# Performance work log

Hardware: AMD Instinct MI355X
Metric: run time of the kernel (lower is better)

## Reference

```python
import jax, jax.numpy as jnp
import numpy as np

SEQ, B, IN, HID = 512, 64, 1024, 1024


def setup_inputs() -> dict:
    key = jax.random.key(0)
    ks = jax.random.split(key, 9)
    scale = 1.0 / np.sqrt(IN + HID)  # ~torch Linear init range
    def lin(k):
        kw, kb = jax.random.split(k)
        W = jax.random.uniform(kw, (IN + HID, HID), jnp.float32, -scale, scale)
        b = jax.random.uniform(kb, (HID,), jnp.float32, -scale, scale)
        return W, b
    W_f, b_f = lin(ks[0])
    W_i, b_i = lin(ks[1])
    W_o, b_o = lin(ks[2])
    W_c, b_c = lin(ks[3])
    x = jax.random.normal(ks[4], (SEQ, B, IN), jnp.float32)
    return {"x": x, "W_f": W_f, "b_f": b_f, "W_i": W_i, "b_i": b_i,
            "W_o": W_o, "b_o": b_o, "W_c": W_c, "b_c": b_c}


def reference(x, W_f, b_f, W_i, b_i, W_o, b_o, W_c, b_c):
    # x: [seq, batch, input_size]; z = concat(hidden, x_t) to match torch.cat((hidden, input[j]), 1)
    batch = x.shape[1]
    hid = W_f.shape[1]
    h0 = jnp.zeros((batch, hid), x.dtype)
    c0 = jnp.zeros((batch, hid), x.dtype)

    def step(carry, xt):
        h, c = carry
        z = jnp.concatenate([h, xt], axis=1)          # [B, hid+in]
        f = jax.nn.sigmoid(z @ W_f + b_f)
        i = jax.nn.sigmoid(z @ W_i + b_i)
        o = jax.nn.sigmoid(z @ W_o + b_o)
        C_hat = jnp.tanh(z @ W_c + b_c)
        c = c * f + C_hat * i
        h = jnp.tanh(c) * o
        return (h, c), h

    (h, c), output = jax.lax.scan(step, (h0, c0), x)  # output: [seq, B, hid]
    return output, h, c
```

## Files before the change

### kernel.cpp

```cpp
#include <hip/hip_runtime.h>
#include <hip/hip_bf16.h>


typedef __attribute__((ext_vector_type(8))) short short8;
typedef __attribute__((ext_vector_type(4))) float f32x4;
typedef __attribute__((ext_vector_type(4))) unsigned int u32x4;

#define SEQ  512
#define NBAT 64
#define RING 128

static __device__ __forceinline__ unsigned short f2b(float f) {
  unsigned u = __float_as_uint(f);
  unsigned r = (u + 0x7fffu + ((u >> 16) & 1u)) >> 16;
  return (unsigned short)r;
}

static __device__ __forceinline__ void gld_lds16(const void* g, void* l) {
  __builtin_amdgcn_global_load_lds((const __attribute__((address_space(1))) void*)g,
                                   (__attribute__((address_space(3))) void*)l, 16, 0, 0);
}
static __device__ __forceinline__ void gld_lds16_sc1(const void* g, void* l) {
  __builtin_amdgcn_global_load_lds((const __attribute__((address_space(1))) void*)g,
                                   (__attribute__((address_space(3))) void*)l, 16, 0, 16);
}

static __device__ __forceinline__ float sigf(float x) { return 1.f / (1.f + __expf(-x)); }
static __device__ __forceinline__ float tanhfast(float x) { return 1.f - 2.f / (1.f + __expf(2.f * x)); }


__global__ __launch_bounds__(512) void pack_w(const float* __restrict__ Wf,
                                              const float* __restrict__ Wi,
                                              const float* __restrict__ Wo,
                                              const float* __restrict__ Wc,
                                              unsigned short* __restrict__ Wht,
                                              unsigned short* __restrict__ Wxt) {
  __shared__ float tile[64][65];
  int bx = blockIdx.x;
  int g  = bx & 3; bx >>= 2;
  int jb = bx & 15;
  int kb = bx >> 4;
  int j0 = jb * 64, k0 = kb * 64;
  const float* W = (g == 0) ? Wf : (g == 1) ? Wi : (g == 2) ? Wo : Wc;
  int t = threadIdx.x;
  {
    int r  = t >> 3;
    int c0 = (t & 7) * 8;
    const float* src = W + (size_t)(k0 + r) * 1024 + j0 + c0;
    float4 a = *(const float4*)src;
    float4 b = *(const float4*)(src + 4);
    tile[r][c0 + 0] = a.x; tile[r][c0 + 1] = a.y; tile[r][c0 + 2] = a.z; tile[r][c0 + 3] = a.w;
    tile[r][c0 + 4] = b.x; tile[r][c0 + 5] = b.y; tile[r][c0 + 6] = b.z; tile[r][c0 + 7] = b.w;
  }
  __syncthreads();
  {
    int jj  = t >> 3;
    int cc8 = t & 7;
    unsigned short v[8];
#pragma unroll
    for (int e = 0; e < 8; ++e) v[e] = f2b(tile[cc8 * 8 + e][jj]);
    size_t p = (size_t)(4 * (j0 + jj) + g);
    if (k0 < 1024)
      *(uint4*)(&Wht[p * 1024 + k0 + cc8 * 8]) = *(const uint4*)v;
    else
      *(uint4*)(&Wxt[p * 1024 + (k0 - 1024) + cc8 * 8]) = *(const uint4*)v;
  }
}

__global__ __launch_bounds__(256) void pack_bias(const float* __restrict__ bf,
                                                 const float* __restrict__ bi,
                                                 const float* __restrict__ bo,
                                                 const float* __restrict__ bc,
                                                 float* __restrict__ bp) {
  int p = blockIdx.x * 256 + threadIdx.x;
  if (p < 4096) {
    int j = p >> 2, g = p & 3;
    const float* b = (g == 0) ? bf : (g == 1) ? bi : (g == 2) ? bo : bc;
    bp[p] = b[j];
  }
}

__global__ __launch_bounds__(256) void conv_x(const float* __restrict__ x,
                                              unsigned short* __restrict__ xb, int n8) {
  int i = blockIdx.x * 256 + threadIdx.x;
  if (i < n8) {
    const float4* xp = (const float4*)x + (size_t)i * 2;
    float4 a = xp[0], b = xp[1];
    unsigned short v[8] = {f2b(a.x), f2b(a.y), f2b(a.z), f2b(a.w),
                           f2b(b.x), f2b(b.y), f2b(b.z), f2b(b.w)};
    *(uint4*)(&xb[(size_t)i * 8]) = *(const uint4*)v;
  }
}

__global__ __launch_bounds__(256) void init_state(unsigned short* __restrict__ hA,
                                                  float* __restrict__ c,
                                                  int* __restrict__ flagw,
                                                  int* __restrict__ gxcnt,
                                                  int* __restrict__ flags4) {
  int i = blockIdx.x * 256 + threadIdx.x;
  if (i < NBAT * 1024) { hA[i] = 0; c[i] = 0.f; }
  if (i < 512) flagw[i] = 0;
  if (i < 256) gxcnt[i] = 0;
  if (i < 4)   flags4[i] = 0;
}


__global__ __launch_bounds__(256, 1) void lstm_fused(
    const unsigned short* __restrict__ Wht,
    const unsigned short* __restrict__ Wxt,
    const float* __restrict__ bp,
    const unsigned short* __restrict__ xb,
    float* __restrict__ GxRing,
    unsigned short* __restrict__ hA,
    unsigned short* __restrict__ hB,
    float* __restrict__ cst,
    float* __restrict__ out,
    float* __restrict__ outH,
    float* __restrict__ outC,
    int* __restrict__ flagw,
    int* __restrict__ gxcnt,
    int* __restrict__ flags4) {
  __shared__ __align__(16) char lds[139584];

  const int tid = threadIdx.x;
  const int bid = blockIdx.x;
  const int lane = tid & 63;

  if (bid < 128) {
    unsigned short* Ws = (unsigned short*)lds;
    char*           Ab = lds + 65536;
    float (*G)[33]     = (float(*)[33])(lds + 131072);

    const int w   = tid >> 6;
    const int w16 = w * 16;
    const int rl  = lane & 15;
    const int kb  = lane >> 4;
    const int p0  = bid * 32;

    {
      const unsigned short* Wsrc = Wht + (size_t)p0 * 1024;
#pragma unroll
      for (int r = 0; r < 16; ++r) {
        int s = r * 256 + tid;
        int row = s >> 7;
        int slot = s & 127;
        int sub = (slot & 7) ^ (row & 7);
        gld_lds16(Wsrc + (size_t)row * 1024 + ((slot & ~7) | sub) * 8,
                  Ws + (size_t)(r * 256 + (tid & 192)) * 8);
      }
    }

    const int gb   = tid >> 2;
    const int gjl  = (tid & 3) * 2;
    const int gidx = gb * 1024 + (p0 >> 2) + gjl;
    float c0 = cst[gidx], c1 = cst[gidx + 1];

    asm volatile("s_waitcnt vmcnt(0)" ::: "memory");
    __syncthreads();

    const int fbase = w * 128;

#define ASTAGE(c_)                                                             \
    {                                                                          \
      const unsigned short* hrow = hsrc + (size_t)w16 * 1024 + (c_) * 128;     \
      char* dbase = Ab + ((c_) & 3) * 16384 + w * 4096;                        \
      _Pragma("unroll") for (int i = 0; i < 4; ++i) {                          \
        int s = i * 64 + lane;                                                 \
        int row_loc = s >> 4;                                                  \
        int slot = s & 15;                                                     \
        int src = slot ^ (row_loc & 7);                                        \
        gld_lds16_sc1(hrow + (size_t)row_loc * 1024 + src * 8,                 \
                      dbase + i * 1024);                                       \
      }                                                                        \
    }

    for (int t = 0; t < SEQ; ++t) {
      const unsigned short* hsrc = (t & 1) ? hB : hA;
      unsigned int*         hdst = (unsigned int*)((t & 1) ? hA : hB);

      {
        while (true) {
          int m0 = __hip_atomic_load(&flagw[fbase + lane * 2],     __ATOMIC_RELAXED, __HIP_MEMORY_SCOPE_AGENT);
          int m1 = __hip_atomic_load(&flagw[fbase + lane * 2 + 1], __ATOMIC_RELAXED, __HIP_MEMORY_SCOPE_AGENT);
          int cg = __hip_atomic_load(&gxcnt[t >> 1],               __ATOMIC_RELAXED, __HIP_MEMORY_SCOPE_AGENT);
          if (__all((m0 >= t) && (m1 >= t) && (cg >= 32))) break;
          __builtin_amdgcn_s_sleep(1);
        }
      }
      __builtin_amdgcn_sched_barrier(0);

      u32x4 gxa, gxb;
      {
        const float* gsrc = GxRing + (size_t)(t & (RING - 1)) * 262144 +
                            (size_t)gb * 4096 + p0 + gjl * 4;
        asm volatile("global_load_dwordx4 %0, %1, off sc1" : "=v"(gxa) : "v"(gsrc));
        asm volatile("global_load_dwordx4 %0, %1, off offset:16 sc1" : "=v"(gxb) : "v"(gsrc));
      }
      __builtin_amdgcn_sched_barrier(0);

      ASTAGE(0); ASTAGE(1); ASTAGE(2); ASTAGE(3);

      f32x4 acc0 = (f32x4){0.f, 0.f, 0.f, 0.f};
      f32x4 acc1 = (f32x4){0.f, 0.f, 0.f, 0.f};

#pragma unroll
      for (int kc = 0; kc < 8; ++kc) {
        if      (kc <= 4) asm volatile("s_waitcnt vmcnt(12)" ::: "memory");
        else if (kc == 5) asm volatile("s_waitcnt vmcnt(8)"  ::: "memory");
        else if (kc == 6) asm volatile("s_waitcnt vmcnt(4)"  ::: "memory");
        else              asm volatile("s_waitcnt vmcnt(0)"  ::: "memory");
        __builtin_amdgcn_sched_barrier(0);
        const char* Abc = Ab + (kc & 3) * 16384 + w * 4096;
#pragma unroll
        for (int ks = 0; ks < 4; ++ks) {
          int g = ks * 4 + kb;
          short8 af = *(const short8*)(Abc + rl * 256 + ((g ^ (rl & 7)) * 16));
          int gslot = kc * 16 + g;
          int gbase = (gslot & ~7) * 16;
          short8 bf0 = *(const short8*)((const char*)Ws + (0 * 16 + rl) * 2048 + gbase +
                                        (((gslot & 7) ^ (rl & 7)) * 16));
          short8 bf1 = *(const short8*)((const char*)Ws + (1 * 16 + rl) * 2048 + gbase +
                                        (((gslot & 7) ^ (rl & 7)) * 16));
          acc0 = __builtin_amdgcn_mfma_f32_16x16x32_bf16(af, bf0, acc0, 0, 0, 0);
          acc1 = __builtin_amdgcn_mfma_f32_16x16x32_bf16(af, bf1, acc1, 0, 0, 0);
        }
        if (kc + 4 < 8) ASTAGE(kc + 4);
      }

#pragma unroll
      for (int r = 0; r < 4; ++r) {
        G[w16 + kb * 4 + r][rl]      = acc0[r];
        G[w16 + kb * 4 + r][16 + rl] = acc1[r];
      }
      f32x4 gx0 = __builtin_bit_cast(f32x4, gxa);
      f32x4 gx1 = __builtin_bit_cast(f32x4, gxb);
      float f0 = sigf(G[gb][gjl * 4 + 0] + gx0[0]);
      float i0 = sigf(G[gb][gjl * 4 + 1] + gx0[1]);
      float o0 = sigf(G[gb][gjl * 4 + 2] + gx0[2]);
      float q0 = tanhfast(G[gb][gjl * 4 + 3] + gx0[3]);
      float f1 = sigf(G[gb][gjl * 4 + 4] + gx1[0]);
      float i1 = sigf(G[gb][gjl * 4 + 5] + gx1[1]);
      float o1 = sigf(G[gb][gjl * 4 + 6] + gx1[2]);
      float q1 = tanhfast(G[gb][gjl * 4 + 7] + gx1[3]);
      c0 = c0 * f0 + q0 * i0;
      c1 = c1 * f1 + q1 * i1;
      float h0 = tanhfast(c0) * o0;
      float h1 = tanhfast(c1) * o1;

      __hip_atomic_store(&hdst[gidx >> 1],
                         ((unsigned)f2b(h1) << 16) | (unsigned)f2b(h0),
                         __ATOMIC_RELAXED, __HIP_MEMORY_SCOPE_AGENT);
      asm volatile("s_waitcnt vmcnt(0)" ::: "memory");
      if (lane == 0) {
        __hip_atomic_store(&flagw[fbase + bid], t + 1, __ATOMIC_RELAXED, __HIP_MEMORY_SCOPE_AGENT);
        if (bid == 0)
          __hip_atomic_store(&flags4[w], t + 1, __ATOMIC_RELAXED, __HIP_MEMORY_SCOPE_AGENT);
      }

      *(float2*)&out[(size_t)t * 65536 + gidx] = make_float2(h0, h1);
      if (t == SEQ - 1) {
        *(float2*)&outH[gidx] = make_float2(h0, h1);
        *(float2*)&outC[gidx] = make_float2(c0, c1);
      }
      asm volatile("s_waitcnt vmcnt(0)" ::: "memory");
    }
#undef ASTAGE

    cst[gidx]     = c0;
    cst[gidx + 1] = c1;

  } else {
    unsigned short* AsW = (unsigned short*)lds;
    unsigned short* BsW = (unsigned short*)(lds + 32768);
    const int wid = bid - 128;
    const int w = tid >> 6;
    const int rl = lane & 15, kb = lane >> 4;
    const int wr = w >> 1, wc = w & 1;

    for (int tau = wid; tau < 8192; tau += 128) {
      int sp = tau >> 5;
      int bn = tau & 31;

      if (2 * sp >= RING - 16) {
        int need = 2 * sp - (RING - 16) + 1;
        while (true) {
          int v = __hip_atomic_load(&flags4[lane & 3], __ATOMIC_RELAXED, __HIP_MEMORY_SCOPE_AGENT);
          if (__all(v >= need)) break;
          __builtin_amdgcn_s_sleep(16);
        }
      }

      const unsigned short* Abase = xb + (size_t)sp * 131072;
      const unsigned short* Bbase = Wxt + (size_t)bn * 131072;

      f32x4 acc[4][4];
#pragma unroll
      for (int m = 0; m < 4; ++m)
#pragma unroll
        for (int n = 0; n < 4; ++n) acc[m][n] = (f32x4){0.f, 0.f, 0.f, 0.f};

#define GSTAGE(k0_, buf_)                                                       \
      {                                                                         \
        _Pragma("unroll") for (int r = 0; r < 4; ++r) {                         \
          int i = r * 256 + tid;                                                \
          int row = i >> 3;                                                     \
          int cc = (i & 7) ^ (row & 7);                                         \
          int base = (r * 256 + (tid & 192)) * 8;                               \
          gld_lds16(Abase + (size_t)row * 1024 + (k0_) + cc * 8, &AsW[(buf_)*8192 + base]); \
          gld_lds16(Bbase + (size_t)row * 1024 + (k0_) + cc * 8, &BsW[(buf_)*8192 + base]); \
        }                                                                       \
      }

      GSTAGE(0, 0);
      __syncthreads();
      int cur = 0;
#pragma unroll 2
      for (int kc = 0; kc < 16; ++kc) {
        if (kc < 15) GSTAGE((kc + 1) * 64, cur ^ 1);
        const char* Abt = (const char*)&AsW[cur * 8192];
        const char* Bbt = (const char*)&BsW[cur * 8192];
#pragma unroll
        for (int ks = 0; ks < 2; ++ks) {
          int g = ks * 4 + kb;
          short8 bf[4], af[4];
#pragma unroll
          for (int nt = 0; nt < 4; ++nt) {
            int brow = wc * 64 + nt * 16 + rl;
            bf[nt] = *(const short8*)(Bbt + brow * 128 + ((g ^ (brow & 7)) * 16));
          }
#pragma unroll
          for (int mt = 0; mt < 4; ++mt) {
            int arow = wr * 64 + mt * 16 + rl;
            af[mt] = *(const short8*)(Abt + arow * 128 + ((g ^ (arow & 7)) * 16));
          }
#pragma unroll
          for (int mt = 0; mt < 4; ++mt)
#pragma unroll
            for (int nt = 0; nt < 4; ++nt)
              acc[mt][nt] = __builtin_amdgcn_mfma_f32_16x16x32_bf16(af[mt], bf[nt], acc[mt][nt], 0, 0, 0);
        }
        __syncthreads();
        cur ^= 1;
      }
#undef GSTAGE

      float* Cb = GxRing + (size_t)((2 * sp) & (RING - 1)) * 262144;
#pragma unroll
      for (int nt = 0; nt < 4; ++nt) {
        int p = bn * 128 + wc * 64 + nt * 16 + rl;
        float bias = bp[p];
#pragma unroll
        for (int mt = 0; mt < 4; ++mt) {
#pragma unroll
          for (int r = 0; r < 4; ++r) {
            int row = wr * 64 + mt * 16 + kb * 4 + r;
            __hip_atomic_store(&Cb[(size_t)row * 4096 + p], acc[mt][nt][r] + bias,
                               __ATOMIC_RELAXED, __HIP_MEMORY_SCOPE_AGENT);
          }
        }
      }
      asm volatile("s_waitcnt vmcnt(0)" ::: "memory");
      __syncthreads();
      if (tid == 0)
        __hip_atomic_fetch_add(&gxcnt[sp], 1, __ATOMIC_RELAXED, __HIP_MEMORY_SCOPE_AGENT);
    }
  }
}


extern "C" void kernel_launch(void* const* d_in, const int* in_sizes, int n_in,
                              void* d_out, int out_size, void* d_ws, size_t ws_size,
                              hipStream_t stream) {
  const float* x  = (const float*)d_in[0];
  const float* Wf = (const float*)d_in[1];
  const float* bf = (const float*)d_in[2];
  const float* Wi = (const float*)d_in[3];
  const float* bi = (const float*)d_in[4];
  const float* Wo = (const float*)d_in[5];
  const float* bo = (const float*)d_in[6];
  const float* Wc = (const float*)d_in[7];
  const float* bc = (const float*)d_in[8];
  float* out = (float*)d_out;

  char* ws = (char*)d_ws;
  unsigned short* Wht = (unsigned short*)(ws);
  unsigned short* Wxt = (unsigned short*)(ws + 8388608);
  float*          bp  = (float*)(ws + 16777216);
  unsigned short* xb  = (unsigned short*)(ws + 16793600);
  unsigned short* hA  = (unsigned short*)(ws + 83902464);
  unsigned short* hB  = (unsigned short*)(ws + 84033536);
  float*          cst = (float*)(ws + 84164608);
  int*            flw = (int*)(ws + 84426752);
  int*            gxc = (int*)(ws + 84430848);
  int*            fl4 = (int*)(ws + 84431872);
  float*          GxR = (float*)(ws + 84440064);

  pack_w    <<<2048,  512, 0, stream>>>(Wf, Wi, Wo, Wc, Wht, Wxt);
  pack_bias <<<16,    256, 0, stream>>>(bf, bi, bo, bc, bp);
  conv_x    <<<16384, 256, 0, stream>>>(x, xb, 4194304);
  init_state<<<256,   256, 0, stream>>>(hA, cst, flw, gxc, fl4);

  float* outH = out + (size_t)SEQ * NBAT * 1024;
  float* outC = outH + NBAT * 1024;

  lstm_fused<<<256, 256, 0, stream>>>(Wht, Wxt, bp, xb, GxR, hA, hB, cst,
                                      out, outH, outC, flw, gxc, fl4);
}
```

Baseline: 2.867 ms.

## Shrink recurrent blocks to 32 with register-resident weights and more Gx workers

The recurrent part now runs on 32 blocks instead of 128. Each block handles 128 gate columns, and each wave keeps its slice of the hidden-to-gate weights in registers (64 short8 values) instead of LDS. Every wave now computes all 64 batch rows against its 32 columns, so it reads the shared h staging buffer, which adds block barriers and reorders when the next h chunks are staged. This cuts the number of blocks that poll each other's flags each step and frees more blocks (224) for the input-projection Gx workers. The cost is very high register pressure, which risks spills, and less parallelism in the serial recurrent path.

```diff
diff --git a/kernel.cpp b/kernel.cpp
--- a/kernel.cpp
+++ b/kernel.cpp
@@ -99,7 +99,7 @@
                                                   int* __restrict__ flags4) {
   int i = blockIdx.x * 256 + threadIdx.x;
   if (i < NBAT * 1024) { hA[i] = 0; c[i] = 0.f; }
-  if (i < 512) flagw[i] = 0;
+  if (i < 128) flagw[i] = 0;
   if (i < 256) gxcnt[i] = 0;
   if (i < 4)   flags4[i] = 0;
 }
@@ -120,49 +120,45 @@
     int* __restrict__ flagw,
     int* __restrict__ gxcnt,
     int* __restrict__ flags4) {
-  __shared__ __align__(16) char lds[139584];
+  __shared__ __align__(16) char lds[98560];
 
   const int tid = threadIdx.x;
   const int bid = blockIdx.x;
   const int lane = tid & 63;
 
-  if (bid < 128) {
-    unsigned short* Ws = (unsigned short*)lds;
-    char*           Ab = lds + 65536;
-    float (*G)[33]     = (float(*)[33])(lds + 131072);
-
-    const int w   = tid >> 6;
-    const int w16 = w * 16;
-    const int rl  = lane & 15;
-    const int kb  = lane >> 4;
-    const int p0  = bid * 32;
-
+  if (bid < 32) {
+    char* Ab        = lds;
+    float (*G)[129] = (float(*)[129])(lds + 65536);
+
+    const int w    = tid >> 6;
+    const int rl   = lane & 15;
+    const int kb   = lane >> 4;
+    const int p0   = bid * 128;
+    const int colb = bid * 32 + w * 8;
+
+    short8 wreg[64];
+#pragma unroll
+    for (int n = 0; n < 2; ++n) {
+      const unsigned short* wp = Wht + (size_t)(p0 + w * 32 + n * 16 + rl) * 1024 + kb * 8;
+#pragma unroll
+      for (int ki = 0; ki < 32; ++ki)
+        wreg[n * 32 + ki] = *(const short8*)(wp + ki * 32);
+    }
+
+    float cr[8];
     {
-      const unsigned short* Wsrc = Wht + (size_t)p0 * 1024;
-#pragma unroll
-      for (int r = 0; r < 16; ++r) {
-        int s = r * 256 + tid;
-        int row = s >> 7;
-        int slot = s & 127;
-        int sub = (slot & 7) ^ (row & 7);
-        gld_lds16(Wsrc + (size_t)row * 1024 + ((slot & ~7) | sub) * 8,
-                  Ws + (size_t)(r * 256 + (tid & 192)) * 8);
-      }
-    }
-
-    const int gb   = tid >> 2;
-    const int gjl  = (tid & 3) * 2;
-    const int gidx = gb * 1024 + (p0 >> 2) + gjl;
-    float c0 = cst[gidx], c1 = cst[gidx + 1];
+      const float* cp = cst + (size_t)lane * 1024 + colb;
+      f32x4 a = *(const f32x4*)cp, b = *(const f32x4*)(cp + 4);
+      cr[0] = a[0]; cr[1] = a[1]; cr[2] = a[2]; cr[3] = a[3];
+      cr[4] = b[0]; cr[5] = b[1]; cr[6] = b[2]; cr[7] = b[3];
+    }
 
     asm volatile("s_waitcnt vmcnt(0)" ::: "memory");
     __syncthreads();
 
-    const int fbase = w * 128;
-
 #define ASTAGE(c_)                                                             \
     {                                                                          \
-      const unsigned short* hrow = hsrc + (size_t)w16 * 1024 + (c_) * 128;     \
+      const unsigned short* hrow = hsrc + (size_t)(w * 16) * 1024 + (c_) * 128;\
       char* dbase = Ab + ((c_) & 3) * 16384 + w * 4096;                        \
       _Pragma("unroll") for (int i = 0; i < 4; ++i) {                          \
         int s = i * 64 + lane;                                                 \
@@ -176,108 +172,148 @@
 
     for (int t = 0; t < SEQ; ++t) {
       const unsigned short* hsrc = (t & 1) ? hB : hA;
-      unsigned int*         hdst = (unsigned int*)((t & 1) ? hA : hB);
+      unsigned short*       hdst = (t & 1) ? hA : hB;
 
       {
         while (true) {
-          int m0 = __hip_atomic_load(&flagw[fbase + lane * 2],     __ATOMIC_RELAXED, __HIP_MEMORY_SCOPE_AGENT);
-          int m1 = __hip_atomic_load(&flagw[fbase + lane * 2 + 1], __ATOMIC_RELAXED, __HIP_MEMORY_SCOPE_AGENT);
-          int cg = __hip_atomic_load(&gxcnt[t >> 1],               __ATOMIC_RELAXED, __HIP_MEMORY_SCOPE_AGENT);
+          int m0 = __hip_atomic_load(&flagw[lane * 2],     __ATOMIC_RELAXED, __HIP_MEMORY_SCOPE_AGENT);
+          int m1 = __hip_atomic_load(&flagw[lane * 2 + 1], __ATOMIC_RELAXED, __HIP_MEMORY_SCOPE_AGENT);
+          int cg = __hip_atomic_load(&gxcnt[t >> 1],       __ATOMIC_RELAXED, __HIP_MEMORY_SCOPE_AGENT);
           if (__all((m0 >= t) && (m1 >= t) && (cg >= 32))) break;
           __builtin_amdgcn_s_sleep(1);
         }
       }
       __builtin_amdgcn_sched_barrier(0);
 
-      u32x4 gxa, gxb;
+      u32x4 gx[8];
       {
         const float* gsrc = GxRing + (size_t)(t & (RING - 1)) * 262144 +
-                            (size_t)gb * 4096 + p0 + gjl * 4;
-        asm volatile("global_load_dwordx4 %0, %1, off sc1" : "=v"(gxa) : "v"(gsrc));
-        asm volatile("global_load_dwordx4 %0, %1, off offset:16 sc1" : "=v"(gxb) : "v"(gsrc));
+                            (size_t)lane * 4096 + p0 + w * 32;
+        asm volatile("global_load_dwordx4 %0, %1, off sc1"           : "=v"(gx[0]) : "v"(gsrc));
+        asm volatile("global_load_dwordx4 %0, %1, off offset:16 sc1" : "=v"(gx[1]) : "v"(gsrc));
+        asm volatile("global_load_dwordx4 %0, %1, off offset:32 sc1" : "=v"(gx[2]) : "v"(gsrc));
+        asm volatile("global_load_dwordx4 %0, %1, off offset:48 sc1" : "=v"(gx[3]) : "v"(gsrc));
+        asm volatile("global_load_dwordx4 %0, %1, off offset:64 sc1" : "=v"(gx[4]) : "v"(gsrc));
+        asm volatile("global_load_dwordx4 %0, %1, off offset:80 sc1" : "=v"(gx[5]) : "v"(gsrc));
+        asm volatile("global_load_dwordx4 %0, %1, off offset:96 sc1" : "=v"(gx[6]) : "v"(gsrc));
+        asm volatile("global_load_dwordx4 %0, %1, off offset:112 sc1": "=v"(gx[7]) : "v"(gsrc));
       }
       __builtin_amdgcn_sched_barrier(0);
 
       ASTAGE(0); ASTAGE(1); ASTAGE(2); ASTAGE(3);
 
-      f32x4 acc0 = (f32x4){0.f, 0.f, 0.f, 0.f};
-      f32x4 acc1 = (f32x4){0.f, 0.f, 0.f, 0.f};
+      f32x4 acc[4][2];
+#pragma unroll
+      for (int mq = 0; mq < 4; ++mq)
+#pragma unroll
+        for (int n = 0; n < 2; ++n) acc[mq][n] = (f32x4){0.f, 0.f, 0.f, 0.f};
 
 #pragma unroll
       for (int kc = 0; kc < 8; ++kc) {
-        if      (kc <= 4) asm volatile("s_waitcnt vmcnt(12)" ::: "memory");
-        else if (kc == 5) asm volatile("s_waitcnt vmcnt(8)"  ::: "memory");
+        if      (kc == 0) asm volatile("s_waitcnt vmcnt(12)" ::: "memory");
+        else if (kc <= 5) asm volatile("s_waitcnt vmcnt(8)"  ::: "memory");
         else if (kc == 6) asm volatile("s_waitcnt vmcnt(4)"  ::: "memory");
         else              asm volatile("s_waitcnt vmcnt(0)"  ::: "memory");
         __builtin_amdgcn_sched_barrier(0);
-        const char* Abc = Ab + (kc & 3) * 16384 + w * 4096;
+        __builtin_amdgcn_s_barrier();
+        __builtin_amdgcn_sched_barrier(0);
+        if (kc >= 1 && kc <= 4) ASTAGE(kc + 3);
+        const char* Abc = Ab + (kc & 3) * 16384;
 #pragma unroll
         for (int ks = 0; ks < 4; ++ks) {
-          int g = ks * 4 + kb;
-          short8 af = *(const short8*)(Abc + rl * 256 + ((g ^ (rl & 7)) * 16));
-          int gslot = kc * 16 + g;
-          int gbase = (gslot & ~7) * 16;
-          short8 bf0 = *(const short8*)((const char*)Ws + (0 * 16 + rl) * 2048 + gbase +
-                                        (((gslot & 7) ^ (rl & 7)) * 16));
-          short8 bf1 = *(const short8*)((const char*)Ws + (1 * 16 + rl) * 2048 + gbase +
-                                        (((gslot & 7) ^ (rl & 7)) * 16));
-          acc0 = __builtin_amdgcn_mfma_f32_16x16x32_bf16(af, bf0, acc0, 0, 0, 0);
-          acc1 = __builtin_amdgcn_mfma_f32_16x16x32_bf16(af, bf1, acc1, 0, 0, 0);
-        }
-        if (kc + 4 < 8) ASTAGE(kc + 4);
-      }
-
-#pragma unroll
-      for (int r = 0; r < 4; ++r) {
-        G[w16 + kb * 4 + r][rl]      = acc0[r];
-        G[w16 + kb * 4 + r][16 + rl] = acc1[r];
-      }
-      f32x4 gx0 = __builtin_bit_cast(f32x4, gxa);
-      f32x4 gx1 = __builtin_bit_cast(f32x4, gxb);
-      float f0 = sigf(G[gb][gjl * 4 + 0] + gx0[0]);
-      float i0 = sigf(G[gb][gjl * 4 + 1] + gx0[1]);
-      float o0 = sigf(G[gb][gjl * 4 + 2] + gx0[2]);
-      float q0 = tanhfast(G[gb][gjl * 4 + 3] + gx0[3]);
-      float f1 = sigf(G[gb][gjl * 4 + 4] + gx1[0]);
-      float i1 = sigf(G[gb][gjl * 4 + 5] + gx1[1]);
-      float o1 = sigf(G[gb][gjl * 4 + 6] + gx1[2]);
-      float q1 = tanhfast(G[gb][gjl * 4 + 7] + gx1[3]);
-      c0 = c0 * f0 + q0 * i0;
-      c1 = c1 * f1 + q1 * i1;
-      float h0 = tanhfast(c0) * o0;
-      float h1 = tanhfast(c1) * o1;
-
-      __hip_atomic_store(&hdst[gidx >> 1],
-                         ((unsigned)f2b(h1) << 16) | (unsigned)f2b(h0),
-                         __ATOMIC_RELAXED, __HIP_MEMORY_SCOPE_AGENT);
+          const int g = ks * 4 + kb;
+          const int ao = rl * 256 + ((g ^ (rl & 7)) * 16);
+          short8 af0 = *(const short8*)(Abc +     0 + ao);
+          short8 af1 = *(const short8*)(Abc +  4096 + ao);
+          short8 af2 = *(const short8*)(Abc +  8192 + ao);
+          short8 af3 = *(const short8*)(Abc + 12288 + ao);
+          const short8 b0 = wreg[kc * 4 + ks];
+          const short8 b1 = wreg[32 + kc * 4 + ks];
+          acc[0][0] = __builtin_amdgcn_mfma_f32_16x16x32_bf16(af0, b0, acc[0][0], 0, 0, 0);
+          acc[0][1] = __builtin_amdgcn_mfma_f32_16x16x32_bf16(af0, b1, acc[0][1], 0, 0, 0);
+          acc[1][0] = __builtin_amdgcn_mfma_f32_16x16x32_bf16(af1, b0, acc[1][0], 0, 0, 0);
+          acc[1][1] = __builtin_amdgcn_mfma_f32_16x16x32_bf16(af1, b1, acc[1][1], 0, 0, 0);
+          acc[2][0] = __builtin_amdgcn_mfma_f32_16x16x32_bf16(af2, b0, acc[2][0], 0, 0, 0);
+          acc[2][1] = __builtin_amdgcn_mfma_f32_16x16x32_bf16(af2, b1, acc[2][1], 0, 0, 0);
+          acc[3][0] = __builtin_amdgcn_mfma_f32_16x16x32_bf16(af3, b0, acc[3][0], 0, 0, 0);
+          acc[3][1] = __builtin_amdgcn_mfma_f32_16x16x32_bf16(af3, b1, acc[3][1], 0, 0, 0);
+        }
+      }
+
+#pragma unroll
+      for (int mq = 0; mq < 4; ++mq)
+#pragma unroll
+        for (int n = 0; n < 2; ++n)
+#pragma unroll
+          for (int r = 0; r < 4; ++r)
+            G[mq * 16 + kb * 4 + r][w * 32 + n * 16 + rl] = acc[mq][n][r];
+
+      float h8[8];
+      {
+        const float* Gr = &G[lane][w * 32];
+#pragma unroll
+        for (int j = 0; j < 8; ++j) {
+          f32x4 q = __builtin_bit_cast(f32x4, gx[j]);
+          float f = sigf(Gr[4 * j + 0] + q[0]);
+          float i = sigf(Gr[4 * j + 1] + q[1]);
+          float o = sigf(Gr[4 * j + 2] + q[2]);
+          float qq = tanhfast(Gr[4 * j + 3] + q[3]);
+          cr[j] = cr[j] * f + qq * i;
+          h8[j] = tanhfast(cr[j]) * o;
+        }
+      }
+
+      {
+        u32x4 hp;
+#pragma unroll
+        for (int d = 0; d < 4; ++d)
+          hp[d] = ((unsigned)f2b(h8[2 * d + 1]) << 16) | (unsigned)f2b(h8[2 * d]);
+        unsigned short* hd = hdst + (size_t)lane * 1024 + colb;
+        asm volatile("global_store_dwordx4 %0, %1, off sc1" :: "v"(hd), "v"(hp) : "memory");
+      }
       asm volatile("s_waitcnt vmcnt(0)" ::: "memory");
       if (lane == 0) {
-        __hip_atomic_store(&flagw[fbase + bid], t + 1, __ATOMIC_RELAXED, __HIP_MEMORY_SCOPE_AGENT);
+        __hip_atomic_store(&flagw[w * 32 + bid], t + 1, __ATOMIC_RELAXED, __HIP_MEMORY_SCOPE_AGENT);
         if (bid == 0)
           __hip_atomic_store(&flags4[w], t + 1, __ATOMIC_RELAXED, __HIP_MEMORY_SCOPE_AGENT);
       }
 
-      *(float2*)&out[(size_t)t * 65536 + gidx] = make_float2(h0, h1);
-      if (t == SEQ - 1) {
-        *(float2*)&outH[gidx] = make_float2(h0, h1);
-        *(float2*)&outC[gidx] = make_float2(c0, c1);
-      }
-      asm volatile("s_waitcnt vmcnt(0)" ::: "memory");
+      {
+        float* op = out + (size_t)t * 65536 + (size_t)lane * 1024 + colb;
+        f32x4 o0, o1;
+        o0[0] = h8[0]; o0[1] = h8[1]; o0[2] = h8[2]; o0[3] = h8[3];
+        o1[0] = h8[4]; o1[1] = h8[5]; o1[2] = h8[6]; o1[3] = h8[7];
+        *(f32x4*)op = o0; *(f32x4*)(op + 4) = o1;
+        if (t == SEQ - 1) {
+          float* hp2 = outH + (size_t)lane * 1024 + colb;
+          float* cp2 = outC + (size_t)lane * 1024 + colb;
+          *(f32x4*)hp2 = o0; *(f32x4*)(hp2 + 4) = o1;
+          f32x4 c0v, c1v;
+          c0v[0] = cr[0]; c0v[1] = cr[1]; c0v[2] = cr[2]; c0v[3] = cr[3];
+          c1v[0] = cr[4]; c1v[1] = cr[5]; c1v[2] = cr[6]; c1v[3] = cr[7];
+          *(f32x4*)cp2 = c0v; *(f32x4*)(cp2 + 4) = c1v;
+        }
+      }
     }
 #undef ASTAGE
 
-    cst[gidx]     = c0;
-    cst[gidx + 1] = c1;
+    {
+      float* cp = cst + (size_t)lane * 1024 + colb;
+      f32x4 c0v, c1v;
+      c0v[0] = cr[0]; c0v[1] = cr[1]; c0v[2] = cr[2]; c0v[3] = cr[3];
+      c1v[0] = cr[4]; c1v[1] = cr[5]; c1v[2] = cr[6]; c1v[3] = cr[7];
+      *(f32x4*)cp = c0v; *(f32x4*)(cp + 4) = c1v;
+    }
 
   } else {
     unsigned short* AsW = (unsigned short*)lds;
     unsigned short* BsW = (unsigned short*)(lds + 32768);
-    const int wid = bid - 128;
+    const int wid = bid - 32;
     const int w = tid >> 6;
     const int rl = lane & 15, kb = lane >> 4;
     const int wr = w >> 1, wc = w & 1;
 
-    for (int tau = wid; tau < 8192; tau += 128) {
+    for (int tau = wid; tau < 8192; tau += 224) {
       int sp = tau >> 5;
       int bn = tau & 31;
 
```

Result: slower. 5.949 ms (+107.5%).

## Halve recurrent blocks by holding extra weight columns in registers

Applied to the files above, without the earlier changes.

The recurrent part now runs on 64 blocks instead of 128, each covering 64 gate columns. Half of each block's weights stay in LDS and the other half are preloaded into 64 short8 registers per thread, which doubles the MFMA work per step. This cuts the number of blocks that must synchronize through flags each timestep and frees 64 extra blocks for the Gx input-projection producers (stride 192). In exchange, every block does twice the serial per-step MFMA and gate math, and register pressure becomes very high, with a risk of spills.

```diff
diff --git a/kernel.cpp b/kernel.cpp
--- a/kernel.cpp
+++ b/kernel.cpp
@@ -5,6 +5,7 @@
 typedef __attribute__((ext_vector_type(8))) short short8;
 typedef __attribute__((ext_vector_type(4))) float f32x4;
 typedef __attribute__((ext_vector_type(4))) unsigned int u32x4;
+typedef __attribute__((ext_vector_type(2))) unsigned int u32x2;
 
 #define SEQ  512
 #define NBAT 64
@@ -99,7 +100,7 @@
                                                   int* __restrict__ flags4) {
   int i = blockIdx.x * 256 + threadIdx.x;
   if (i < NBAT * 1024) { hA[i] = 0; c[i] = 0.f; }
-  if (i < 512) flagw[i] = 0;
+  if (i < 256) flagw[i] = 0;
   if (i < 256) gxcnt[i] = 0;
   if (i < 4)   flags4[i] = 0;
 }
@@ -120,22 +121,22 @@
     int* __restrict__ flagw,
     int* __restrict__ gxcnt,
     int* __restrict__ flags4) {
-  __shared__ __align__(16) char lds[139584];
+  __shared__ __align__(16) char lds[147712];
 
   const int tid = threadIdx.x;
   const int bid = blockIdx.x;
   const int lane = tid & 63;
 
-  if (bid < 128) {
+  if (bid < 64) {
     unsigned short* Ws = (unsigned short*)lds;
     char*           Ab = lds + 65536;
-    float (*G)[33]     = (float(*)[33])(lds + 131072);
+    float (*G)[65]     = (float(*)[65])(lds + 131072);
 
     const int w   = tid >> 6;
     const int w16 = w * 16;
     const int rl  = lane & 15;
     const int kb  = lane >> 4;
-    const int p0  = bid * 32;
+    const int p0  = bid * 64;
 
     {
       const unsigned short* Wsrc = Wht + (size_t)p0 * 1024;
@@ -150,15 +151,26 @@
       }
     }
 
+    short8 wreg[64];
+#pragma unroll
+    for (int n = 0; n < 2; ++n) {
+      const unsigned short* wp = Wht + (size_t)(p0 + 32 + n * 16 + rl) * 1024 + kb * 8;
+#pragma unroll
+      for (int ki = 0; ki < 32; ++ki)
+        wreg[n * 32 + ki] = *(const short8*)(wp + ki * 32);
+    }
+
     const int gb   = tid >> 2;
-    const int gjl  = (tid & 3) * 2;
-    const int gidx = gb * 1024 + (p0 >> 2) + gjl;
-    float c0 = cst[gidx], c1 = cst[gidx + 1];
+    const int tl   = tid & 3;
+    const int gidx = gb * 1024 + bid * 16 + tl * 4;
+    float cr[4];
+    {
+      f32x4 cv = *(const f32x4*)(cst + gidx);
+      cr[0] = cv[0]; cr[1] = cv[1]; cr[2] = cv[2]; cr[3] = cv[3];
+    }
 
     asm volatile("s_waitcnt vmcnt(0)" ::: "memory");
     __syncthreads();
-
-    const int fbase = w * 128;
 
 #define ASTAGE(c_)                                                             \
     {                                                                          \
@@ -176,25 +188,26 @@
 
     for (int t = 0; t < SEQ; ++t) {
       const unsigned short* hsrc = (t & 1) ? hB : hA;
-      unsigned int*         hdst = (unsigned int*)((t & 1) ? hA : hB);
+      unsigned short*       hdst = (t & 1) ? hA : hB;
 
       {
         while (true) {
-          int m0 = __hip_atomic_load(&flagw[fbase + lane * 2],     __ATOMIC_RELAXED, __HIP_MEMORY_SCOPE_AGENT);
-          int m1 = __hip_atomic_load(&flagw[fbase + lane * 2 + 1], __ATOMIC_RELAXED, __HIP_MEMORY_SCOPE_AGENT);
-          int cg = __hip_atomic_load(&gxcnt[t >> 1],               __ATOMIC_RELAXED, __HIP_MEMORY_SCOPE_AGENT);
-          if (__all((m0 >= t) && (m1 >= t) && (cg >= 32))) break;
+          int m  = __hip_atomic_load(&flagw[w * 64 + lane], __ATOMIC_RELAXED, __HIP_MEMORY_SCOPE_AGENT);
+          int cg = __hip_atomic_load(&gxcnt[t >> 1],        __ATOMIC_RELAXED, __HIP_MEMORY_SCOPE_AGENT);
+          if (__all((m >= t) && (cg >= 32))) break;
           __builtin_amdgcn_s_sleep(1);
         }
       }
       __builtin_amdgcn_sched_barrier(0);
 
-      u32x4 gxa, gxb;
+      u32x4 gx0, gx1, gx2, gx3;
       {
         const float* gsrc = GxRing + (size_t)(t & (RING - 1)) * 262144 +
-                            (size_t)gb * 4096 + p0 + gjl * 4;
-        asm volatile("global_load_dwordx4 %0, %1, off sc1" : "=v"(gxa) : "v"(gsrc));
-        asm volatile("global_load_dwordx4 %0, %1, off offset:16 sc1" : "=v"(gxb) : "v"(gsrc));
+                            (size_t)gb * 4096 + p0 + tl * 16;
+        asm volatile("global_load_dwordx4 %0, %1, off sc1"           : "=v"(gx0) : "v"(gsrc));
+        asm volatile("global_load_dwordx4 %0, %1, off offset:16 sc1" : "=v"(gx1) : "v"(gsrc));
+        asm volatile("global_load_dwordx4 %0, %1, off offset:32 sc1" : "=v"(gx2) : "v"(gsrc));
+        asm volatile("global_load_dwordx4 %0, %1, off offset:48 sc1" : "=v"(gx3) : "v"(gsrc));
       }
       __builtin_amdgcn_sched_barrier(0);
 
@@ -202,6 +215,8 @@
 
       f32x4 acc0 = (f32x4){0.f, 0.f, 0.f, 0.f};
       f32x4 acc1 = (f32x4){0.f, 0.f, 0.f, 0.f};
+      f32x4 acc2 = (f32x4){0.f, 0.f, 0.f, 0.f};
+      f32x4 acc3 = (f32x4){0.f, 0.f, 0.f, 0.f};
 
 #pragma unroll
       for (int kc = 0; kc < 8; ++kc) {
@@ -221,63 +236,84 @@
                                         (((gslot & 7) ^ (rl & 7)) * 16));
           short8 bf1 = *(const short8*)((const char*)Ws + (1 * 16 + rl) * 2048 + gbase +
                                         (((gslot & 7) ^ (rl & 7)) * 16));
+          const short8 b2 = wreg[kc * 4 + ks];
+          const short8 b3 = wreg[32 + kc * 4 + ks];
           acc0 = __builtin_amdgcn_mfma_f32_16x16x32_bf16(af, bf0, acc0, 0, 0, 0);
           acc1 = __builtin_amdgcn_mfma_f32_16x16x32_bf16(af, bf1, acc1, 0, 0, 0);
+          acc2 = __builtin_amdgcn_mfma_f32_16x16x32_bf16(af, b2,  acc2, 0, 0, 0);
+          acc3 = __builtin_amdgcn_mfma_f32_16x16x32_bf16(af, b3,  acc3, 0, 0, 0);
         }
         if (kc + 4 < 8) ASTAGE(kc + 4);
       }
 
 #pragma unroll
       for (int r = 0; r < 4; ++r) {
-        G[w16 + kb * 4 + r][rl]      = acc0[r];
+        G[w16 + kb * 4 + r][ 0 + rl] = acc0[r];
         G[w16 + kb * 4 + r][16 + rl] = acc1[r];
-      }
-      f32x4 gx0 = __builtin_bit_cast(f32x4, gxa);
-      f32x4 gx1 = __builtin_bit_cast(f32x4, gxb);
-      float f0 = sigf(G[gb][gjl * 4 + 0] + gx0[0]);
-      float i0 = sigf(G[gb][gjl * 4 + 1] + gx0[1]);
-      float o0 = sigf(G[gb][gjl * 4 + 2] + gx0[2]);
-      float q0 = tanhfast(G[gb][gjl * 4 + 3] + gx0[3]);
-      float f1 = sigf(G[gb][gjl * 4 + 4] + gx1[0]);
-      float i1 = sigf(G[gb][gjl * 4 + 5] + gx1[1]);
-      float o1 = sigf(G[gb][gjl * 4 + 6] + gx1[2]);
-      float q1 = tanhfast(G[gb][gjl * 4 + 7] + gx1[3]);
-      c0 = c0 * f0 + q0 * i0;
-      c1 = c1 * f1 + q1 * i1;
-      float h0 = tanhfast(c0) * o0;
-      float h1 = tanhfast(c1) * o1;
-
-      __hip_atomic_store(&hdst[gidx >> 1],
-                         ((unsigned)f2b(h1) << 16) | (unsigned)f2b(h0),
-                         __ATOMIC_RELAXED, __HIP_MEMORY_SCOPE_AGENT);
+        G[w16 + kb * 4 + r][32 + rl] = acc2[r];
+        G[w16 + kb * 4 + r][48 + rl] = acc3[r];
+      }
+
+      float h4[4];
+      {
+        const float* Gr = &G[gb][tl * 16];
+        f32x4 q0 = __builtin_bit_cast(f32x4, gx0);
+        f32x4 q1 = __builtin_bit_cast(f32x4, gx1);
+        f32x4 q2 = __builtin_bit_cast(f32x4, gx2);
+        f32x4 q3 = __builtin_bit_cast(f32x4, gx3);
+        float f, i, o, qq;
+        f = sigf(Gr[ 0] + q0[0]); i = sigf(Gr[ 1] + q0[1]); o = sigf(Gr[ 2] + q0[2]); qq = tanhfast(Gr[ 3] + q0[3]);
+        cr[0] = cr[0] * f + qq * i;  h4[0] = tanhfast(cr[0]) * o;
+        f = sigf(Gr[ 4] + q1[0]); i = sigf(Gr[ 5] + q1[1]); o = sigf(Gr[ 6] + q1[2]); qq = tanhfast(Gr[ 7] + q1[3]);
+        cr[1] = cr[1] * f + qq * i;  h4[1] = tanhfast(cr[1]) * o;
+        f = sigf(Gr[ 8] + q2[0]); i = sigf(Gr[ 9] + q2[1]); o = sigf(Gr[10] + q2[2]); qq = tanhfast(Gr[11] + q2[3]);
+        cr[2] = cr[2] * f + qq * i;  h4[2] = tanhfast(cr[2]) * o;
+        f = sigf(Gr[12] + q3[0]); i = sigf(Gr[13] + q3[1]); o = sigf(Gr[14] + q3[2]); qq = tanhfast(Gr[15] + q3[3]);
+        cr[3] = cr[3] * f + qq * i;  h4[3] = tanhfast(cr[3]) * o;
+      }
+
+      {
+        u32x2 hp;
+        hp[0] = ((unsigned)f2b(h4[1]) << 16) | (unsigned)f2b(h4[0]);
+        hp[1] = ((unsigned)f2b(h4[3]) << 16) | (unsigned)f2b(h4[2]);
+        unsigned short* hd = hdst + gidx;
+        asm volatile("global_store_dwordx2 %0, %1, off sc1" :: "v"(hd), "v"(hp) : "memory");
+      }
       asm volatile("s_waitcnt vmcnt(0)" ::: "memory");
       if (lane == 0) {
-        __hip_atomic_store(&flagw[fbase + bid], t + 1, __ATOMIC_RELAXED, __HIP_MEMORY_SCOPE_AGENT);
+        __hip_atomic_store(&flagw[w * 64 + bid], t + 1, __ATOMIC_RELAXED, __HIP_MEMORY_SCOPE_AGENT);
         if (bid == 0)
           __hip_atomic_store(&flags4[w], t + 1, __ATOMIC_RELAXED, __HIP_MEMORY_SCOPE_AGENT);
       }
 
-      *(float2*)&out[(size_t)t * 65536 + gidx] = make_float2(h0, h1);
-      if (t == SEQ - 1) {
-        *(float2*)&outH[gidx] = make_float2(h0, h1);
-        *(float2*)&outC[gidx] = make_float2(c0, c1);
+      {
+        f32x4 o0;
+        o0[0] = h4[0]; o0[1] = h4[1]; o0[2] = h4[2]; o0[3] = h4[3];
+        *(f32x4*)&out[(size_t)t * 65536 + gidx] = o0;
+        if (t == SEQ - 1) {
+          *(f32x4*)&outH[gidx] = o0;
+          f32x4 cv; cv[0] = cr[0]; cv[1] = cr[1]; cv[2] = cr[2]; cv[3] = cr[3];
+          *(f32x4*)&outC[gidx] = cv;
+        }
       }
       asm volatile("s_waitcnt vmcnt(0)" ::: "memory");
     }
 #undef ASTAGE
 
-    cst[gidx]     = c0;
-    cst[gidx + 1] = c1;
+    {
+      f32x4 cv; cv[0] = cr[0]; cv[1] = cr[1]; cv[2] = cr[2]; cv[3] = cr[3];
+      *(f32x4*)&cst[gidx] = cv;
+    }
 
   } else {
     unsigned short* AsW = (unsigned short*)lds;
     unsigned short* BsW = (unsigned short*)(lds + 32768);
-    const int wid = bid - 128;
+    const int wid = bid - 64;
     const int w = tid >> 6;
     const int rl = lane & 15, kb = lane >> 4;
     const int wr = w >> 1, wc = w & 1;
 
-    for (int tau = wid; tau < 8192; tau += 128) {
+    for (int tau = wid; tau < 8192; tau += 192) {
       int sp = tau >> 5;
       int bn = tau & 31;
 
```

Result: slower. 3.346 ms (+16.7%).

## Keep recurrent weight slice in registers and stage all h chunks up front

Applied to the files above, without the earlier changes.

Each block's slice of the recurrent weight is now loaded once into registers (64 short8 per lane) instead of into LDS, so the inner MFMA loop reads only the h operand from LDS. The freed LDS lets all eight h chunks be issued at once into distinct buffers, and the waitcnt ladder is extended to match. This removes per-step LDS reads of the weights and the rolling four-buffer restaging, in exchange for very high VGPR pressure that may cause spills or reduce occupancy.

```diff
diff --git a/kernel.cpp b/kernel.cpp
--- a/kernel.cpp
+++ b/kernel.cpp
@@ -127,8 +127,7 @@
   const int lane = tid & 63;
 
   if (bid < 128) {
-    unsigned short* Ws = (unsigned short*)lds;
-    char*           Ab = lds + 65536;
+    char*           Ab = lds;
     float (*G)[33]     = (float(*)[33])(lds + 131072);
 
     const int w   = tid >> 6;
@@ -137,16 +136,14 @@
     const int kb  = lane >> 4;
     const int p0  = bid * 32;
 
+    short8 wr0[32], wr1[32];
     {
-      const unsigned short* Wsrc = Wht + (size_t)p0 * 1024;
-#pragma unroll
-      for (int r = 0; r < 16; ++r) {
-        int s = r * 256 + tid;
-        int row = s >> 7;
-        int slot = s & 127;
-        int sub = (slot & 7) ^ (row & 7);
-        gld_lds16(Wsrc + (size_t)row * 1024 + ((slot & ~7) | sub) * 8,
-                  Ws + (size_t)(r * 256 + (tid & 192)) * 8);
+      const unsigned short* wp0 = Wht + (size_t)(p0 +      rl) * 1024 + kb * 8;
+      const unsigned short* wp1 = Wht + (size_t)(p0 + 16 + rl) * 1024 + kb * 8;
+#pragma unroll
+      for (int ki = 0; ki < 32; ++ki) {
+        wr0[ki] = *(const short8*)(wp0 + ki * 32);
+        wr1[ki] = *(const short8*)(wp1 + ki * 32);
       }
     }
 
@@ -163,7 +160,7 @@
 #define ASTAGE(c_)                                                             \
     {                                                                          \
       const unsigned short* hrow = hsrc + (size_t)w16 * 1024 + (c_) * 128;     \
-      char* dbase = Ab + ((c_) & 3) * 16384 + w * 4096;                        \
+      char* dbase = Ab + (c_) * 16384 + w * 4096;                              \
       _Pragma("unroll") for (int i = 0; i < 4; ++i) {                          \
         int s = i * 64 + lane;                                                 \
         int row_loc = s >> 4;                                                  \
@@ -199,32 +196,30 @@
       __builtin_amdgcn_sched_barrier(0);
 
       ASTAGE(0); ASTAGE(1); ASTAGE(2); ASTAGE(3);
+      ASTAGE(4); ASTAGE(5); ASTAGE(6); ASTAGE(7);
 
       f32x4 acc0 = (f32x4){0.f, 0.f, 0.f, 0.f};
       f32x4 acc1 = (f32x4){0.f, 0.f, 0.f, 0.f};
 
 #pragma unroll
       for (int kc = 0; kc < 8; ++kc) {
-        if      (kc <= 4) asm volatile("s_waitcnt vmcnt(12)" ::: "memory");
+        if      (kc == 0) asm volatile("s_waitcnt vmcnt(28)" ::: "memory");
+        else if (kc == 1) asm volatile("s_waitcnt vmcnt(24)" ::: "memory");
+        else if (kc == 2) asm volatile("s_waitcnt vmcnt(20)" ::: "memory");
+        else if (kc == 3) asm volatile("s_waitcnt vmcnt(16)" ::: "memory");
+        else if (kc == 4) asm volatile("s_waitcnt vmcnt(12)" ::: "memory");
         else if (kc == 5) asm volatile("s_waitcnt vmcnt(8)"  ::: "memory");
         else if (kc == 6) asm volatile("s_waitcnt vmcnt(4)"  ::: "memory");
         else              asm volatile("s_waitcnt vmcnt(0)"  ::: "memory");
         __builtin_amdgcn_sched_barrier(0);
-        const char* Abc = Ab + (kc & 3) * 16384 + w * 4096;
+        const char* Abc = Ab + kc * 16384 + w * 4096;
 #pragma unroll
         for (int ks = 0; ks < 4; ++ks) {
           int g = ks * 4 + kb;
           short8 af = *(const short8*)(Abc + rl * 256 + ((g ^ (rl & 7)) * 16));
-          int gslot = kc * 16 + g;
-          int gbase = (gslot & ~7) * 16;
-          short8 bf0 = *(const short8*)((const char*)Ws + (0 * 16 + rl) * 2048 + gbase +
-                                        (((gslot & 7) ^ (rl & 7)) * 16));
-          short8 bf1 = *(const short8*)((const char*)Ws + (1 * 16 + rl) * 2048 + gbase +
-                                        (((gslot & 7) ^ (rl & 7)) * 16));
-          acc0 = __builtin_amdgcn_mfma_f32_16x16x32_bf16(af, bf0, acc0, 0, 0, 0);
-          acc1 = __builtin_amdgcn_mfma_f32_16x16x32_bf16(af, bf1, acc1, 0, 0, 0);
+          acc0 = __builtin_amdgcn_mfma_f32_16x16x32_bf16(af, wr0[kc * 4 + ks], acc0, 0, 0, 0);
+          acc1 = __builtin_amdgcn_mfma_f32_16x16x32_bf16(af, wr1[kc * 4 + ks], acc1, 0, 0, 0);
         }
-        if (kc + 4 < 8) ASTAGE(kc + 4);
       }
 
 #pragma unroll
```

Result: slower. 3.085 ms (+7.6%).
